# Kernel tuning notes

Hardware: AMD Instinct MI355X
Metric: run time of the kernel (lower is better)

## Reference

```python
import jax, jax.numpy as jnp
import numpy as np

N, SEQ, HID, ENC, E = 16384, 512, 1024, 256, 8


def setup_inputs() -> dict:
    key = jax.random.key(0)
    ks = jax.random.split(key, 8)
    def w(k, shape, fan_in):
        return jax.random.normal(k, shape, dtype=jnp.float32) * (1.0 / np.sqrt(fan_in))
    return {
        "x": jax.random.normal(ks[0], (N, SEQ), dtype=jnp.float32),
        "ids": jax.random.randint(ks[1], (N,), 0, E),
        "W1": w(ks[2], (SEQ, HID), SEQ),
        "b1": jnp.zeros((HID,), jnp.float32),
        "W2": w(ks[3], (HID, ENC), HID),
        "b2": jnp.zeros((ENC,), jnp.float32),
        "W3": w(ks[4], (E, ENC, HID), ENC),
        "b3": jnp.zeros((E, HID), jnp.float32),
        "W4": w(ks[5], (E, HID, SEQ), HID),
        "b4": jnp.zeros((E, SEQ), jnp.float32),
    }


def reference(x, ids, W1, b1, W2, b2, W3, b3, W4, b4):
    # fixed trunk (shared across all combination IDs)
    h = jax.nn.relu(x @ W1 + b1)          # [N, HID]
    z = jax.nn.relu(h @ W2 + b2)          # [N, ENC]
    # per-combination expert head: Linear(enc,hid)+ReLU+Linear(hid,seq)
    n_experts = W3.shape[0]
    oh = jax.nn.one_hot(ids, n_experts, dtype=x.dtype)  # [N, E] row->expert mask
    y = jnp.zeros((x.shape[0], W4.shape[-1]), dtype=x.dtype)
    for e in range(n_experts):  # small fixed expert count; each iter is a big GEMM
        u = jax.nn.relu(z @ W3[e] + b3[e])             # [N, HID]
        y = y + (u @ W4[e] + b4[e]) * oh[:, e:e + 1]   # scatter-back via mask
    return y
```

## Files before the change

### kernel.cpp

```cpp
#include <hip/hip_runtime.h>
#include <hip/hip_bf16.h>

#define NROWS 16384
#define SEQD  512
#define HIDD  1024
#define ENCD  256
#define NEXP  8
#define NBLK  64
#define MAXTILES 136
#define MPAD_MAX (MAXTILES * 128)

using bf16 = __hip_bfloat16;
typedef __bf16 bf16x8 __attribute__((ext_vector_type(8)));
typedef float  f32x4  __attribute__((ext_vector_type(4)));

enum : size_t {
  OFF_XB   = 0,
  OFF_W1T  = OFF_XB  + (size_t)NROWS * SEQD * 2,
  OFF_W2T  = OFF_W1T + (size_t)HIDD * SEQD * 2,
  OFF_H    = OFF_W2T + (size_t)ENCD * HIDD * 2,
  OFF_W3T  = OFF_H   + (size_t)NROWS * HIDD * 2,
  OFF_W4T  = OFF_W3T + (size_t)NEXP * HIDD * ENCD * 2,
  OFF_Z    = OFF_W4T + (size_t)NEXP * SEQD * HIDD * 2,
  OFF_PERM = OFF_Z   + (size_t)NROWS * ENCD * 2,
  OFF_META = OFF_PERM + (size_t)MPAD_MAX * 4,
  OFF_U    = 0,
  WS_NEED  = OFF_META + 8192
};

__device__ __forceinline__ void gload_lds16(const void* g, void* l) {
  __builtin_amdgcn_global_load_lds(
      (const __attribute__((address_space(1))) void*)g,
      (__attribute__((address_space(3))) void*)l, 16, 0, 0);
}

__global__ void prep_k(const float* __restrict__ x,
                       const float* __restrict__ W1, const float* __restrict__ W2,
                       const float* __restrict__ W3, const float* __restrict__ W4,
                       bf16* __restrict__ Xb, bf16* __restrict__ W1t,
                       bf16* __restrict__ W2t, bf16* __restrict__ W3t,
                       bf16* __restrict__ W4t) {
  __shared__ float t[32][33];
  int b = blockIdx.x;
  const int tid = threadIdx.x;
  if (b < 4096) {
    size_t i = (size_t)b * 256 + tid;
    float4 a = ((const float4*)x)[i * 2];
    float4 c = ((const float4*)x)[i * 2 + 1];
    __align__(16) bf16 v[8] = {
      __float2bfloat16(a.x), __float2bfloat16(a.y), __float2bfloat16(a.z), __float2bfloat16(a.w),
      __float2bfloat16(c.x), __float2bfloat16(c.y), __float2bfloat16(c.z), __float2bfloat16(c.w)};
    *(int4*)(Xb + i * 8) = *(const int4*)v;
    return;
  }
  b -= 4096;
  const float* s; bf16* d; int R, C;
  if (b < 512)              { s = W1; d = W1t; R = SEQD; C = HIDD; }
  else if ((b -= 512) < 256){ s = W2; d = W2t; R = HIDD; C = ENCD; }
  else if ((b -= 256) < 2048){
    int z = b >> 8; b &= 255; s = W3 + (size_t)z * ENCD * HIDD; d = W3t + (size_t)z * ENCD * HIDD;
    R = ENCD; C = HIDD;
  } else {
    b -= 2048; int z = b >> 9; b &= 511;
    s = W4 + (size_t)z * HIDD * SEQD; d = W4t + (size_t)z * HIDD * SEQD;
    R = HIDD; C = SEQD;
  }
  const int nbx = C >> 5;
  const int bx = (b % nbx) * 32, by = (b / nbx) * 32;
  const int tx = tid & 31, ty = tid >> 5;
  #pragma unroll
  for (int i = 0; i < 32; i += 8) t[ty + i][tx] = s[(size_t)(by + ty + i) * C + bx + tx];
  __syncthreads();
  #pragma unroll
  for (int i = 0; i < 32; i += 8)
    d[(size_t)(bx + ty + i) * R + by + tx] = __float2bfloat16(t[tx][ty + i]);
}


__global__ void count_k(const int* __restrict__ ids, int* __restrict__ gh) {
  __shared__ int c[NEXP];
  const int tid = threadIdx.x;
  if (tid < NEXP) c[tid] = 0;
  __syncthreads();
  atomicAdd(&c[ids[blockIdx.x * 256 + tid]], 1);
  __syncthreads();
  if (tid < NEXP) gh[blockIdx.x * NEXP + tid] = c[tid];
}

__global__ __launch_bounds__(1024) void bases_k(int* __restrict__ meta,
                                                int* __restrict__ perm) {
  int* gh        = meta;
  int* bases     = meta + 512;
  int* blockbase = meta + 528;
  __shared__ int counts[NEXP];
  __shared__ int base_s[NEXP + 1];
  const int tid = threadIdx.x;
  if (tid < NEXP) {
    int s = 0;
    for (int b = 0; b < NBLK; ++b) s += gh[b * NEXP + tid];
    counts[tid] = s;
  }
  __syncthreads();
  if (tid == 0) {
    int t = 0;
    for (int e = 0; e < NEXP; ++e) { base_s[e] = t; t += (counts[e] + 127) & ~127; }
    base_s[NEXP] = t;
  }
  __syncthreads();
  if (tid < NEXP) {
    int run = base_s[tid];
    for (int b = 0; b < NBLK; ++b) { blockbase[b * NEXP + tid] = run; run += gh[b * NEXP + tid]; }
  }
  if (tid == 0)
    for (int e = 0; e <= NEXP; ++e) bases[e] = base_s[e];
  #pragma unroll
  for (int e = 0; e < NEXP; ++e) {
    int lo = base_s[e] + counts[e];
    int i  = lo + tid;
    if (i < base_s[e + 1]) perm[i] = -1;
  }
}

__global__ void scatter_k(const int* __restrict__ ids, const int* __restrict__ blockbase,
                          int* __restrict__ perm) {
  __shared__ int wavehist[4][NEXP];
  const int tid = threadIdx.x, w = tid >> 6, lane = tid & 63;
  const int n = blockIdx.x * 256 + tid;
  const int e = ids[n];
  const unsigned long long lt = (1ull << lane) - 1ull;
  int myrank = 0;
  #pragma unroll
  for (int ee = 0; ee < NEXP; ++ee) {
    unsigned long long bb = __ballot(e == ee);
    if (ee == e) myrank = __popcll(bb & lt);
    if (lane == 0) wavehist[w][ee] = __popcll(bb);
  }
  __syncthreads();
  int pre = 0;
  for (int w2 = 0; w2 < w; ++w2) pre += wavehist[w2][e];
  perm[blockbase[blockIdx.x * NEXP + e] + pre + myrank] = n;
}

template <bool GATHER_A, bool EXPERT, bool RELU, bool SCATTER_F32>
__global__ __launch_bounds__(256) void gemm128(
    const bf16* __restrict__ A, const bf16* __restrict__ Bt,
    const float* __restrict__ bias, void* __restrict__ Out,
    int Ncols, int K, const int* __restrict__ perm, const int* __restrict__ bases) {
  __shared__ char As[16384];
  __shared__ char Bs[16384];

  const int tid  = threadIdx.x;
  const int wid  = tid >> 6;
  const int lane = tid & 63;
  const int lm = lane & 15, l4 = lane >> 4;
  const int wm = wid >> 1, wn = wid & 1;

  const int tileM = blockIdx.x, tileN = blockIdx.y;
  int expert = 0;
  if (EXPERT) {
    const int total = bases[8];
    if (tileM * 128 >= total) return;
    const int r0 = tileM * 128;
    #pragma unroll
    for (int e = 1; e < NEXP; ++e) expert += (r0 >= bases[e]) ? 1 : 0;
    Bt   += (size_t)expert * Ncols * K;
    bias += expert * Ncols;
  }
  const int row0 = tileM * 128, col0 = tileN * 128;

  const bf16* gA[4];
  const bf16* gB[4];
  #pragma unroll
  for (int i = 0; i < 4; ++i) {
    int flat = (i * 4 + wid) * 1024 + lane * 16;
    int r    = flat >> 7;
    int cb   = (flat & 127) ^ ((r & 7) << 4);
    int arow;
    if (GATHER_A) {
      int p = perm[row0 + r];
      arow = (p < 0) ? 0 : p;
    } else {
      arow = row0 + r;
    }
    gA[i] = A  + (size_t)arow * K + (cb >> 1);
    gB[i] = Bt + (size_t)(col0 + r) * K + (cb >> 1);
  }

  f32x4 acc[4][4];
  #pragma unroll
  for (int i = 0; i < 4; ++i)
    #pragma unroll
    for (int j = 0; j < 4; ++j) { f32x4 z = {0.f, 0.f, 0.f, 0.f}; acc[i][j] = z; }

  int aoff[4], boff[4];
  const int swz = (lm & 7) << 4;
  #pragma unroll
  for (int i = 0; i < 4; ++i) {
    int ar = wm * 64 + i * 16 + lm;
    aoff[i] = ar * 128 + ((l4 * 16) ^ swz);
    int br = wn * 64 + i * 16 + lm;
    boff[i] = br * 128 + ((l4 * 16) ^ swz);
  }

  const int nk = K >> 6;
  for (int kt = 0; kt < nk; ++kt) {
    #pragma unroll
    for (int i = 0; i < 4; ++i) {
      gload_lds16(gA[i] + kt * 64, As + (i * 4 + wid) * 1024);
      gload_lds16(gB[i] + kt * 64, Bs + (i * 4 + wid) * 1024);
    }
    __syncthreads();
    #pragma unroll
    for (int kk = 0; kk < 2; ++kk) {
      bf16x8 af[4], bfr[4];
      #pragma unroll
      for (int i = 0; i < 4; ++i) af[i]  = *(const bf16x8*)(As + (aoff[i] ^ (kk * 64)));
      #pragma unroll
      for (int i = 0; i < 4; ++i) bfr[i] = *(const bf16x8*)(Bs + (boff[i] ^ (kk * 64)));
      #pragma unroll
      for (int mi = 0; mi < 4; ++mi)
        #pragma unroll
        for (int ni = 0; ni < 4; ++ni)
          acc[mi][ni] = __builtin_amdgcn_mfma_f32_16x16x32_bf16(af[mi], bfr[ni], acc[mi][ni], 0, 0, 0);
    }
    __syncthreads();
  }

  float bv[4];
  #pragma unroll
  for (int ni = 0; ni < 4; ++ni) bv[ni] = bias[col0 + wn * 64 + ni * 16 + lm];
  #pragma unroll
  for (int mi = 0; mi < 4; ++mi) {
    #pragma unroll
    for (int r = 0; r < 4; ++r) {
      int rowp = row0 + wm * 64 + mi * 16 + l4 * 4 + r;
      int orow = rowp;
      bool valid = true;
      if (SCATTER_F32) {
        int p = perm[rowp];
        valid = (p >= 0);
        orow  = valid ? p : 0;
      }
      #pragma unroll
      for (int ni = 0; ni < 4; ++ni) {
        float v = acc[mi][ni][r] + bv[ni];
        if (RELU) v = v > 0.f ? v : 0.f;
        int n = col0 + wn * 64 + ni * 16 + lm;
        if (SCATTER_F32) {
          if (valid) ((float*)Out)[(size_t)orow * Ncols + n] = v;
        } else {
          ((bf16*)Out)[(size_t)rowp * Ncols + n] = __float2bfloat16(v);
        }
      }
    }
  }
}

extern "C" void kernel_launch(void* const* d_in, const int* in_sizes, int n_in,
                              void* d_out, int out_size, void* d_ws, size_t ws_size,
                              hipStream_t stream) {
  const float* x  = (const float*)d_in[0];
  const int*   ids= (const int*)d_in[1];
  const float* W1 = (const float*)d_in[2];
  const float* b1 = (const float*)d_in[3];
  const float* W2 = (const float*)d_in[4];
  const float* b2 = (const float*)d_in[5];
  const float* W3 = (const float*)d_in[6];
  const float* b3 = (const float*)d_in[7];
  const float* W4 = (const float*)d_in[8];
  const float* b4 = (const float*)d_in[9];

  char* ws = (char*)d_ws;
  bf16* Xb  = (bf16*)(ws + OFF_XB);
  bf16* W1t = (bf16*)(ws + OFF_W1T);
  bf16* W2t = (bf16*)(ws + OFF_W2T);
  bf16* W3t = (bf16*)(ws + OFF_W3T);
  bf16* W4t = (bf16*)(ws + OFF_W4T);
  bf16* H   = (bf16*)(ws + OFF_H);
  bf16* Z   = (bf16*)(ws + OFF_Z);
  bf16* U   = (bf16*)(ws + OFF_U);
  int*  perm      = (int*)(ws + OFF_PERM);
  int*  meta      = (int*)(ws + OFF_META);
  int*  gh        = meta;
  int*  bases     = meta + 512;
  int*  blockbase = meta + 528;

  prep_k<<<dim3(11008), dim3(256), 0, stream>>>(x, W1, W2, W3, W4, Xb, W1t, W2t, W3t, W4t);
  count_k  <<<dim3(NBLK), dim3(256), 0, stream>>>(ids, gh);
  bases_k  <<<dim3(1),    dim3(1024), 0, stream>>>(meta, perm);
  scatter_k<<<dim3(NBLK), dim3(256), 0, stream>>>(ids, blockbase, perm);

  gemm128<false, false, true, false><<<dim3(NROWS / 128, HIDD / 128), dim3(256), 0, stream>>>(
      Xb, W1t, b1, H, HIDD, SEQD, nullptr, nullptr);
  gemm128<false, false, true, false><<<dim3(NROWS / 128, ENCD / 128), dim3(256), 0, stream>>>(
      H, W2t, b2, Z, ENCD, HIDD, nullptr, nullptr);
  gemm128<true, true, true, false><<<dim3(MAXTILES, HIDD / 128), dim3(256), 0, stream>>>(
      Z, W3t, b3, U, HIDD, ENCD, perm, bases);
  gemm128<false, true, false, true><<<dim3(MAXTILES, SEQD / 128), dim3(256), 0, stream>>>(
      U, W4t, b4, d_out, SEQD, HIDD, perm, bases);

  (void)in_sizes; (void)n_in; (void)out_size; (void)ws_size;
}
```

Before: 128.2 us.

## Double-buffer LDS tiles with async global-to-LDS prefetch two stages ahead

Replaces the single-buffered A/B shared tiles with a 64KB two-stage ring. The next two K-tiles are issued as direct global-to-LDS loads, and the loop waits with s_waitcnt vmcnt(8) so that MFMA compute on one stage overlaps the memory fetch of the other. It also adds a min-2-blocks occupancy hint, but 64KB of LDS per block may limit how many blocks fit per CU, and the hand-placed barriers and waitcnts have to be correct for the data to be valid.

```diff
diff --git a/kernel.cpp b/kernel.cpp
--- a/kernel.cpp
+++ b/kernel.cpp
@@ -142,12 +142,11 @@
 }
 
 template <bool GATHER_A, bool EXPERT, bool RELU, bool SCATTER_F32>
-__global__ __launch_bounds__(256) void gemm128(
+__global__ __launch_bounds__(256, 2) void gemm128(
     const bf16* __restrict__ A, const bf16* __restrict__ Bt,
     const float* __restrict__ bias, void* __restrict__ Out,
     int Ncols, int K, const int* __restrict__ perm, const int* __restrict__ bases) {
-  __shared__ char As[16384];
-  __shared__ char Bs[16384];
+  __shared__ char lds[65536];
 
   const int tid  = threadIdx.x;
   const int wid  = tid >> 6;
@@ -203,28 +202,55 @@
   }
 
   const int nk = K >> 6;
+  const int ldsoff = (wid * 4) * 1024 + (lane & 3) * 16 + ((lane >> 2) << 8);
+  asm volatile("s_waitcnt vmcnt(0)" ::: "memory");
+  __builtin_amdgcn_sched_barrier(0);
+
+  #pragma unroll
+  for (int i = 0; i < 4; ++i) {
+    gload_lds16(gA[i], lds + (i * 4 + wid) * 1024);
+    gload_lds16(gB[i], lds + 16384 + (i * 4 + wid) * 1024);
+  }
+  #pragma unroll
+  for (int i = 0; i < 4; ++i) {
+    gload_lds16(gA[i] + 64, lds + 32768 + (i * 4 + wid) * 1024);
+    gload_lds16(gB[i] + 64, lds + 32768 + 16384 + (i * 4 + wid) * 1024);
+  }
+
   for (int kt = 0; kt < nk; ++kt) {
-    #pragma unroll
-    for (int i = 0; i < 4; ++i) {
-      gload_lds16(gA[i] + kt * 64, As + (i * 4 + wid) * 1024);
-      gload_lds16(gB[i] + kt * 64, Bs + (i * 4 + wid) * 1024);
-    }
-    __syncthreads();
+    if (kt < nk - 1) asm volatile("s_waitcnt vmcnt(8)" ::: "memory");
+    else             asm volatile("s_waitcnt vmcnt(0)" ::: "memory");
+    asm volatile("s_barrier" ::: "memory");
+    __builtin_amdgcn_sched_barrier(0);
+
+    const char* Ac = lds + (kt & 1) * 32768;
+    const char* Bc = Ac + 16384;
     #pragma unroll
     for (int kk = 0; kk < 2; ++kk) {
       bf16x8 af[4], bfr[4];
       #pragma unroll
-      for (int i = 0; i < 4; ++i) af[i]  = *(const bf16x8*)(As + (aoff[i] ^ (kk * 64)));
-      #pragma unroll
-      for (int i = 0; i < 4; ++i) bfr[i] = *(const bf16x8*)(Bs + (boff[i] ^ (kk * 64)));
+      for (int i = 0; i < 4; ++i) af[i]  = *(const bf16x8*)(Ac + (aoff[i] ^ (kk * 64)));
+      #pragma unroll
+      for (int i = 0; i < 4; ++i) bfr[i] = *(const bf16x8*)(Bc + (boff[i] ^ (kk * 64)));
       #pragma unroll
       for (int mi = 0; mi < 4; ++mi)
         #pragma unroll
         for (int ni = 0; ni < 4; ++ni)
           acc[mi][ni] = __builtin_amdgcn_mfma_f32_16x16x32_bf16(af[mi], bfr[ni], acc[mi][ni], 0, 0, 0);
     }
-    __syncthreads();
-  }
+
+    asm volatile("s_barrier" ::: "memory");
+    __builtin_amdgcn_sched_barrier(0);
+    if (kt + 2 < nk) {
+      char* An = lds + (kt & 1) * 32768;
+      #pragma unroll
+      for (int i = 0; i < 4; ++i) {
+        gload_lds16(gA[i] + (size_t)(kt + 2) * 64, An + (i * 4 + wid) * 1024);
+        gload_lds16(gB[i] + (size_t)(kt + 2) * 64, An + 16384 + (i * 4 + wid) * 1024);
+      }
+    }
+  }
+  (void)ldsoff;
 
   float bv[4];
   #pragma unroll
```

Measured after the change: 119.4 us. 6.9% less time.
